# Optimization experiments

Hardware: AMD Instinct MI355X
Metric: run time of the kernel (lower is better)

Reference implementation:

```python
import jax, jax.numpy as jnp
import numpy as np

B, SW, SS, D, H = 2, 1024, 256, 1024, 16  # D = hidden_dim*num_heads = 64*16


def _dense_init(key, d_in, d_out):
    # xavier_uniform kernel, zero bias
    lim = np.sqrt(6.0 / (d_in + d_out))
    k = jax.random.uniform(key, (d_in, d_out), jnp.float32, -lim, lim)
    b = jnp.zeros((d_out,), jnp.float32)
    return k, b


def setup_inputs() -> dict:
    key = jax.random.key(0)
    ks = jax.random.split(key, 16)
    inp = {
        'word_inputs': jax.random.normal(ks[0], (B, SW, D), jnp.float32),
        'word_context': jax.random.normal(ks[1], (B, SW, D), jnp.float32),
        'sentence_inputs': jax.random.normal(ks[2], (B, SS, D), jnp.float32),
        'sentence_context': jax.random.normal(ks[3], (B, SS, D), jnp.float32),
        'word_mask': jax.random.uniform(ks[4], (B, H, SW, SW), jnp.float32),
        'sentence_mask': jax.random.uniform(ks[5], (B, H, SS, SS), jnp.float32),
    }
    names = ['wq', 'wk', 'wv', 'wo', 'sq', 'sk', 'sv', 'so']
    for i, n in enumerate(names):
        kk, bb = _dense_init(ks[6 + i], D, D)
        inp[n + '_k'] = kk
        inp[n + '_b'] = bb
    return inp


def _attention(q, k, v, mask):
    # Faithful to source: split heads by raw reshape (B, H, L, hd),
    # scale by sqrt(full key dim), multiplicative mask.
    Bq, Lk, Dm = v.shape[0], v.shape[1], q.shape[-1]
    hd = Dm // H
    qh = jnp.reshape(q, (Bq, H, Lk, hd))
    kh = jnp.reshape(k, (Bq, H, Lk, hd))
    vh = jnp.reshape(v, (Bq, H, Lk, hd))
    scores = jnp.einsum('bhqd,bhkd->bhqk', qh, kh) / jnp.sqrt(jnp.float32(Dm))
    if mask is not None:
        scores = scores * mask
    attn = jax.nn.softmax(scores, axis=-1)
    ctx = jnp.einsum('bhqk,bhkd->bhqd', attn, vh)
    return attn, jnp.reshape(ctx, (Bq, Lk, Dm))


def reference(word_inputs, word_context, sentence_inputs, sentence_context,
              word_mask, sentence_mask,
              wq_k, wq_b, wk_k, wk_b, wv_k, wv_b, wo_k, wo_b,
              sq_k, sq_b, sk_k, sk_b, sv_k, sv_b, so_k, so_b):
    dense = lambda x, k, b: jnp.einsum('bld,de->ble', x, k) + b
    wq = dense(word_inputs, wq_k, wq_b)
    wk = dense(word_context, wk_k, wk_b)
    wv = dense(word_context, wv_k, wv_b)
    word_attn, word_ctx = _attention(wq, wk, wv, word_mask)
    sq = dense(sentence_inputs, sq_k, sq_b)
    sk = dense(sentence_context, sk_k, sk_b)
    sv = dense(sentence_context, sv_k, sv_b)
    sent_attn, sent_ctx = _attention(sq, sk, sv, sentence_mask)
    word_out = dense(word_ctx, wo_k, wo_b)
    sent_out = dense(sent_ctx, so_k, so_b)
    return (word_out, sent_out, word_attn, sent_attn)
```

## Files before the change

### kernel.cpp

```cpp
#include <hip/hip_runtime.h>
#include <hip/hip_bf16.h>
#include <stdint.h>

typedef __attribute__((ext_vector_type(8))) short short8;
typedef __attribute__((ext_vector_type(4))) float f32x4;

__device__ __forceinline__ f32x4 mfma16(short8 a, short8 b, f32x4 c){
  return __builtin_amdgcn_mfma_f32_16x16x32_bf16(a, b, c, 0, 0, 0);
}

union BF8 { short8 v; __hip_bfloat16 h[8]; };

__device__ __forceinline__ void gld_lds16(const void* g, void* l){
  __builtin_amdgcn_global_load_lds((const __attribute__((address_space(1))) void*)g,
                                   (__attribute__((address_space(3))) void*)l, 16, 0, 0);
}

struct GemmDesc { const __hip_bfloat16* A; const __hip_bfloat16* W; const float* bias; void* out; int M; float scale; };
struct GemmArgs { GemmDesc d[6]; };
struct PrepWArgs { const float* src[8]; };
struct CvtArgs { const float* src[4]; __hip_bfloat16* dst[4]; int n[4]; };

__global__ __launch_bounds__(256) void cvt_k(CvtArgs c){
  int z = blockIdx.z;
  int n = c.n[z];
  int i = (blockIdx.x * 256 + threadIdx.x) * 8;
  if (i >= n) return;
  const float4* s = (const float4*)(c.src[z] + i);
  float4 u0 = s[0], u1 = s[1];
  BF8 cv;
  cv.h[0] = __float2bfloat16(u0.x); cv.h[1] = __float2bfloat16(u0.y);
  cv.h[2] = __float2bfloat16(u0.z); cv.h[3] = __float2bfloat16(u0.w);
  cv.h[4] = __float2bfloat16(u1.x); cv.h[5] = __float2bfloat16(u1.y);
  cv.h[6] = __float2bfloat16(u1.z); cv.h[7] = __float2bfloat16(u1.w);
  *(short8*)(c.dst[z] + i) = cv.v;
}

__global__ __launch_bounds__(256) void prep_w_k(PrepWArgs pa, __hip_bfloat16* dst){
  __shared__ float t[64][65];
  const float* W = pa.src[blockIdx.z];
  int k0 = blockIdx.y * 64, n0 = blockIdx.x * 64;
  int c = threadIdx.x & 63, r0 = (threadIdx.x >> 6) * 16;
  #pragma unroll
  for (int i = 0; i < 16; ++i) t[r0 + i][c] = W[(size_t)(k0 + r0 + i) * 1024 + n0 + c];
  __syncthreads();
  __hip_bfloat16* D = dst + (size_t)blockIdx.z * 1048576;
  #pragma unroll
  for (int i = 0; i < 16; ++i) D[(size_t)(n0 + r0 + i) * 1024 + k0 + c] = __float2bfloat16(t[c][r0 + i]);
}

__global__ __launch_bounds__(256) void prep_v_k(const __hip_bfloat16* vw, const __hip_bfloat16* vs,
                                                __hip_bfloat16* vtw, __hip_bfloat16* vts){
  bool word = (blockIdx.z == 0);
  int L = word ? 1024 : 256;
  if (!word && blockIdx.x >= 4) return;
  __shared__ __hip_bfloat16 t[64][65];
  const __hip_bfloat16* src = (word ? vw : vs) + (size_t)blockIdx.y * L * 64;
  __hip_bfloat16* dst = (word ? vtw : vts) + (size_t)blockIdx.y * L * 64;
  int l0 = blockIdx.x * 64;
  int c = threadIdx.x & 63, r0 = (threadIdx.x >> 6) * 16;
  #pragma unroll
  for (int i = 0; i < 16; ++i) t[r0 + i][c] = src[(size_t)(l0 + r0 + i) * 64 + c];
  __syncthreads();
  #pragma unroll
  for (int i = 0; i < 16; ++i) dst[(size_t)(r0 + i) * L + l0 + c] = t[c][r0 + i];
}

template<bool OUT_BF16>
__global__ __launch_bounds__(256) void gemm_k(GemmArgs ga){
  GemmDesc dd = ga.d[blockIdx.z];
  int m0 = blockIdx.y * 128;
  if (m0 >= dd.M) return;
  int n0 = blockIdx.x * 128;

  __shared__ __align__(16) __hip_bfloat16 lA[2][128 * 32];
  __shared__ __align__(16) __hip_bfloat16 lB[2][128 * 32];

  int tid = threadIdx.x, lane = tid & 63, wv = tid >> 6;
  int r16 = lane & 15, g = lane >> 4;
  int wr = wv >> 1, wc = wv & 1;

  const __hip_bfloat16* Ab = dd.A + (size_t)m0 * 1024;
  const __hip_bfloat16* Wb = dd.W + (size_t)n0 * 1024;
  int lrow = lane >> 2;
  int scol = (lane & 3) * 8;

  #define STAGE(buf, kc)                                                            \
    {                                                                               \
      _Pragma("unroll")                                                             \
      for (int h = 0; h < 2; ++h){                                                  \
        int rbase = h * 64 + wv * 16;                                               \
        int row = rbase + lrow;                                                     \
        gld_lds16(Ab + (size_t)row * 1024 + (kc) + scol, &lA[buf][rbase * 32]);     \
        gld_lds16(Wb + (size_t)row * 1024 + (kc) + scol, &lB[buf][rbase * 32]);     \
      }                                                                             \
    }

  f32x4 acc[4][4] = {};
  STAGE(0, 0);
  int cur = 0;
  for (int kc = 0; kc < 1024; kc += 32){
    if (kc + 32 < 1024) STAGE(cur ^ 1, kc + 32);
    __syncthreads();
    const __hip_bfloat16* la = &lA[cur][(wr * 64) * 32];
    const __hip_bfloat16* lb = &lB[cur][(wc * 64) * 32];
    short8 af[4], bfr[4];
    #pragma unroll
    for (int t = 0; t < 4; ++t){
      af[t]  = *(const short8*)(la + (t * 16 + r16) * 32 + g * 8);
      bfr[t] = *(const short8*)(lb + (t * 16 + r16) * 32 + g * 8);
    }
    #pragma unroll
    for (int mt = 0; mt < 4; ++mt)
      #pragma unroll
      for (int nt = 0; nt < 4; ++nt)
        acc[mt][nt] = mfma16(af[mt], bfr[nt], acc[mt][nt]);
    __syncthreads();
    cur ^= 1;
  }
  #undef STAGE

  #pragma unroll
  for (int nt = 0; nt < 4; ++nt){
    int col = n0 + wc * 64 + nt * 16 + r16;
    float bb = dd.bias[col];
    #pragma unroll
    for (int mt = 0; mt < 4; ++mt){
      int row0 = m0 + wr * 64 + mt * 16 + g * 4;
      #pragma unroll
      for (int r = 0; r < 4; ++r){
        float v = (acc[mt][nt][r] + bb) * dd.scale;
        if (OUT_BF16) ((__hip_bfloat16*)dd.out)[(size_t)(row0 + r) * 1024 + col] = __float2bfloat16(v);
        else          ((float*)dd.out)[(size_t)(row0 + r) * 1024 + col] = v;
      }
    }
  }
}

template<int L>
__global__ __launch_bounds__(512, 3) void attn_k(
    const __hip_bfloat16* __restrict__ qb, const __hip_bfloat16* __restrict__ kb,
    const __hip_bfloat16* __restrict__ vt, const float* __restrict__ mask,
    float* __restrict__ attn, __hip_bfloat16* __restrict__ ctx){
  constexpr int KQ = L / 4, KT = KQ / 16, CH = KQ / 32;
  int bh = blockIdx.y;
  int q0 = blockIdx.x * 32;
  int lane = threadIdx.x & 63, wv = threadIdx.x >> 6;
  int qt = wv >> 2, kq = wv & 3;
  int r16 = lane & 15, g = lane >> 4;
  size_t ho = (size_t)bh * L * 64;
  const __hip_bfloat16* Qp = qb + ho;
  const __hip_bfloat16* Kp = kb + ho + (size_t)kq * KQ * 64;
  const __hip_bfloat16* Vp = vt + ho;
  int q = q0 + qt * 16 + r16;
  const float* mrow = mask + (size_t)bh * L * L + (size_t)q * L + kq * KQ;
  float* arow = attn + (size_t)bh * L * L + (size_t)q * L + kq * KQ;

  short8 qf0 = *(const short8*)(Qp + (size_t)q * 64 + g * 8);
  short8 qf1 = *(const short8*)(Qp + (size_t)q * 64 + 32 + g * 8);

  f32x4 s[KT];
  #pragma unroll
  for (int kt = 0; kt < KT; ++kt){
    const __hip_bfloat16* kr = Kp + (size_t)(kt * 16 + r16) * 64 + g * 8;
    short8 kf0 = *(const short8*)kr;
    short8 kf1 = *(const short8*)(kr + 32);
    f32x4 t = {};
    t = mfma16(kf0, qf0, t);
    t = mfma16(kf1, qf1, t);
    float4 mv = *(const float4*)(mrow + kt * 16 + g * 4);
    t[0] *= mv.x; t[1] *= mv.y; t[2] *= mv.z; t[3] *= mv.w;
    s[kt] = t;
  }

  float mx = -3.0e38f;
  #pragma unroll
  for (int kt = 0; kt < KT; ++kt)
    #pragma unroll
    for (int r = 0; r < 4; ++r) mx = fmaxf(mx, s[kt][r]);
  mx = fmaxf(mx, __shfl_xor(mx, 16));
  mx = fmaxf(mx, __shfl_xor(mx, 32));
  __shared__ float redm[2][4][16], redl[2][4][16];
  if (lane < 16) redm[qt][kq][lane] = mx;
  __syncthreads();
  mx = fmaxf(fmaxf(redm[qt][0][r16], redm[qt][1][r16]),
             fmaxf(redm[qt][2][r16], redm[qt][3][r16]));
  float sm = 0.f;
  #pragma unroll
  for (int kt = 0; kt < KT; ++kt)
    #pragma unroll
    for (int r = 0; r < 4; ++r){ float e = __expf(s[kt][r] - mx); s[kt][r] = e; sm += e; }
  sm += __shfl_xor(sm, 16);
  sm += __shfl_xor(sm, 32);
  if (lane < 16) redl[qt][kq][lane] = sm;
  __syncthreads();
  sm = (redl[qt][0][r16] + redl[qt][1][r16]) + (redl[qt][2][r16] + redl[qt][3][r16]);
  float inv = 1.0f / sm;

  #pragma unroll
  for (int kt = 0; kt < KT; ++kt){
    float4 v;
    v.x = s[kt][0] * inv; v.y = s[kt][1] * inv;
    v.z = s[kt][2] * inv; v.w = s[kt][3] * inv;
    s[kt][0] = v.x; s[kt][1] = v.y; s[kt][2] = v.z; s[kt][3] = v.w;
    *(float4*)(arow + kt * 16 + g * 4) = v;
  }

  __shared__ __align__(16) __hip_bfloat16 plds[8][16][40];
  f32x4 c4[4] = {};
  #pragma unroll
  for (int ch = 0; ch < CH; ++ch){
    asm volatile("s_waitcnt lgkmcnt(0)" ::: "memory");
    #pragma unroll
    for (int t = 0; t < 2; ++t){
      union { uint64_t u; __hip_bfloat16 h[4]; } pk;
      pk.h[0] = __float2bfloat16(s[2 * ch + t][0]);
      pk.h[1] = __float2bfloat16(s[2 * ch + t][1]);
      pk.h[2] = __float2bfloat16(s[2 * ch + t][2]);
      pk.h[3] = __float2bfloat16(s[2 * ch + t][3]);
      *(uint64_t*)&plds[wv][r16][t * 16 + g * 4] = pk.u;
    }
    asm volatile("s_waitcnt lgkmcnt(0)" ::: "memory");
    __builtin_amdgcn_sched_barrier(0);
    short8 pf = *(const short8*)&plds[wv][r16][g * 8];
    const __hip_bfloat16* vpp = Vp + kq * KQ + ch * 32 + g * 8;
    #pragma unroll
    for (int nt = 0; nt < 4; ++nt){
      short8 vf = *(const short8*)(vpp + (size_t)(nt * 16 + r16) * L);
      c4[nt] = mfma16(pf, vf, c4[nt]);
    }
  }

  __shared__ float ctxl[2][4][16][65];
  #pragma unroll
  for (int nt = 0; nt < 4; ++nt)
    #pragma unroll
    for (int r = 0; r < 4; ++r) ctxl[qt][kq][g * 4 + r][nt * 16 + r16] = c4[nt][r];
  __syncthreads();
  {
    int dq = kq * 16 + g * 4;
    union { uint64_t u; __hip_bfloat16 h[4]; } ov;
    #pragma unroll
    for (int rr = 0; rr < 4; ++rr){
      float v = (ctxl[qt][0][r16][dq + rr] + ctxl[qt][1][r16][dq + rr]) +
                (ctxl[qt][2][r16][dq + rr] + ctxl[qt][3][r16][dq + rr]);
      ov.h[rr] = __float2bfloat16(v);
    }
    *(uint64_t*)(ctx + ho + (size_t)(q0 + qt * 16 + r16) * 64 + dq) = ov.u;
  }
}

extern "C" void kernel_launch(void* const* d_in, const int* in_sizes, int n_in,
                              void* d_out, int out_size, void* d_ws, size_t ws_size,
                              hipStream_t stream){
  const float* word_mask = (const float*)d_in[4];
  const float* sent_mask = (const float*)d_in[5];

  char* ws = (char*)d_ws;
  const size_t MB = 1048576;
  __hip_bfloat16* Wt   = (__hip_bfloat16*)(ws);
  __hip_bfloat16* bwi  = (__hip_bfloat16*)(ws + 16 * MB);
  __hip_bfloat16* bwc  = (__hip_bfloat16*)(ws + 20 * MB);
  __hip_bfloat16* bsi  = (__hip_bfloat16*)(ws + 24 * MB);
  __hip_bfloat16* bsc  = (__hip_bfloat16*)(ws + 25 * MB);
  __hip_bfloat16* qw   = (__hip_bfloat16*)(ws + 26 * MB);
  __hip_bfloat16* kw   = (__hip_bfloat16*)(ws + 30 * MB);
  __hip_bfloat16* vw   = (__hip_bfloat16*)(ws + 34 * MB);
  __hip_bfloat16* sqb  = (__hip_bfloat16*)(ws + 38 * MB);
  __hip_bfloat16* skb  = (__hip_bfloat16*)(ws + 39 * MB);
  __hip_bfloat16* svb  = (__hip_bfloat16*)(ws + 40 * MB);
  __hip_bfloat16* vtw  = (__hip_bfloat16*)(ws + 41 * MB);
  __hip_bfloat16* vts  = (__hip_bfloat16*)(ws + 45 * MB);
  __hip_bfloat16* ctxw = (__hip_bfloat16*)(ws + 46 * MB);
  __hip_bfloat16* ctxs = (__hip_bfloat16*)(ws + 50 * MB);

  float* out = (float*)d_out;
  float* word_out  = out;
  float* sent_out  = out + 2097152;
  float* word_attn = out + 2621440;
  float* sent_attn = out + 36175872;

  PrepWArgs pw;
  pw.src[0] = (const float*)d_in[6];  pw.src[1] = (const float*)d_in[8];
  pw.src[2] = (const float*)d_in[10]; pw.src[3] = (const float*)d_in[12];
  pw.src[4] = (const float*)d_in[14]; pw.src[5] = (const float*)d_in[16];
  pw.src[6] = (const float*)d_in[18]; pw.src[7] = (const float*)d_in[20];
  prep_w_k<<<dim3(16, 16, 8), 256, 0, stream>>>(pw, Wt);

  CvtArgs cv;
  cv.src[0] = (const float*)d_in[0]; cv.dst[0] = bwi; cv.n[0] = 2097152;
  cv.src[1] = (const float*)d_in[1]; cv.dst[1] = bwc; cv.n[1] = 2097152;
  cv.src[2] = (const float*)d_in[2]; cv.dst[2] = bsi; cv.n[2] = 524288;
  cv.src[3] = (const float*)d_in[3]; cv.dst[3] = bsc; cv.n[3] = 524288;
  cvt_k<<<dim3(1024, 1, 4), 256, 0, stream>>>(cv);

  GemmArgs g1;
  g1.d[0] = { bwi, Wt + (size_t)0 * 1048576, (const float*)d_in[7],  qw,  2048, 1.0f / 32.0f };
  g1.d[1] = { bwc, Wt + (size_t)1 * 1048576, (const float*)d_in[9],  kw,  2048, 1.0f };
  g1.d[2] = { bwc, Wt + (size_t)2 * 1048576, (const float*)d_in[11], vw,  2048, 1.0f };
  g1.d[3] = { bsi, Wt + (size_t)4 * 1048576, (const float*)d_in[15], sqb, 512,  1.0f / 32.0f };
  g1.d[4] = { bsc, Wt + (size_t)5 * 1048576, (const float*)d_in[17], skb, 512,  1.0f };
  g1.d[5] = { bsc, Wt + (size_t)6 * 1048576, (const float*)d_in[19], svb, 512,  1.0f };
  gemm_k<true><<<dim3(8, 16, 6), 256, 0, stream>>>(g1);

  prep_v_k<<<dim3(16, 32, 2), 256, 0, stream>>>(vw, svb, vtw, vts);

  attn_k<1024><<<dim3(32, 32), 512, 0, stream>>>(qw, kw, vtw, word_mask, word_attn, ctxw);
  attn_k<256><<<dim3(8, 32), 512, 0, stream>>>(sqb, skb, vts, sent_mask, sent_attn, ctxs);

  GemmArgs g2 = {};
  g2.d[0] = { ctxw, Wt + (size_t)3 * 1048576, (const float*)d_in[13], word_out, 2048, 1.0f };
  g2.d[1] = { ctxs, Wt + (size_t)7 * 1048576, (const float*)d_in[21], sent_out, 512,  1.0f };
  gemm_k<false><<<dim3(8, 16, 2), 256, 0, stream>>>(g2);
}
```

Baseline: 200.4 us.

## Software-pipeline K, mask and V loads in attention kernel

Restructures the attention kernel's QK^T loop to prefetch K fragments four tiles ahead in a ring buffer and batch mask loads in groups of eight. The PV loop double-buffers V fragments one chunk ahead and drops the explicit lgkmcnt waits and sched barrier around the LDS round-trip. Occupancy hint drops from 3 to 2 blocks per SM to make room for the extra registers. The goal is to hide global load latency; risks are register pressure, lower occupancy, and relying on the compiler to order the LDS write and read correctly.

```diff
diff --git a/kernel.cpp b/kernel.cpp
--- a/kernel.cpp
+++ b/kernel.cpp
@@ -138,11 +138,12 @@
 }
 
 template<int L>
-__global__ __launch_bounds__(512, 3) void attn_k(
+__global__ __launch_bounds__(512, 2) void attn_k(
     const __hip_bfloat16* __restrict__ qb, const __hip_bfloat16* __restrict__ kb,
     const __hip_bfloat16* __restrict__ vt, const float* __restrict__ mask,
     float* __restrict__ attn, __hip_bfloat16* __restrict__ ctx){
   constexpr int KQ = L / 4, KT = KQ / 16, CH = KQ / 32;
+  constexpr int MC = (KT < 8) ? KT : 8;
   int bh = blockIdx.y;
   int q0 = blockIdx.x * 32;
   int lane = threadIdx.x & 63, wv = threadIdx.x >> 6;
@@ -160,17 +161,34 @@
   short8 qf1 = *(const short8*)(Qp + (size_t)q * 64 + 32 + g * 8);
 
   f32x4 s[KT];
-  #pragma unroll
-  for (int kt = 0; kt < KT; ++kt){
-    const __hip_bfloat16* kr = Kp + (size_t)(kt * 16 + r16) * 64 + g * 8;
-    short8 kf0 = *(const short8*)kr;
-    short8 kf1 = *(const short8*)(kr + 32);
-    f32x4 t = {};
-    t = mfma16(kf0, qf0, t);
-    t = mfma16(kf1, qf1, t);
-    float4 mv = *(const float4*)(mrow + kt * 16 + g * 4);
-    t[0] *= mv.x; t[1] *= mv.y; t[2] *= mv.z; t[3] *= mv.w;
-    s[kt] = t;
+  short8 kfa[4], kfb[4];
+  #pragma unroll
+  for (int p = 0; p < 4 && p < KT; ++p){
+    const __hip_bfloat16* kr = Kp + (size_t)(p * 16 + r16) * 64 + g * 8;
+    kfa[p] = *(const short8*)kr;
+    kfb[p] = *(const short8*)(kr + 32);
+  }
+  #pragma unroll
+  for (int h2 = 0; h2 < KT / MC; ++h2){
+    float4 mv[MC];
+    #pragma unroll
+    for (int j = 0; j < MC; ++j)
+      mv[j] = *(const float4*)(mrow + (h2 * MC + j) * 16 + g * 4);
+    #pragma unroll
+    for (int j = 0; j < MC; ++j){
+      int kt = h2 * MC + j;
+      short8 a0 = kfa[kt & 3], a1 = kfb[kt & 3];
+      if (kt + 4 < KT){
+        const __hip_bfloat16* kr = Kp + (size_t)((kt + 4) * 16 + r16) * 64 + g * 8;
+        kfa[kt & 3] = *(const short8*)kr;
+        kfb[kt & 3] = *(const short8*)(kr + 32);
+      }
+      f32x4 t = {};
+      t = mfma16(a0, qf0, t);
+      t = mfma16(a1, qf1, t);
+      t[0] *= mv[j].x; t[1] *= mv[j].y; t[2] *= mv[j].z; t[3] *= mv[j].w;
+      s[kt] = t;
+    }
   }
 
   float mx = -3.0e38f;
@@ -208,9 +226,18 @@
 
   __shared__ __align__(16) __hip_bfloat16 plds[8][16][40];
   f32x4 c4[4] = {};
+  const __hip_bfloat16* vbase = Vp + kq * KQ;
+  short8 vf0[4], vf1[4];
+  #pragma unroll
+  for (int nt = 0; nt < 4; ++nt)
+    vf0[nt] = *(const short8*)(vbase + (size_t)(nt * 16 + r16) * L + g * 8);
   #pragma unroll
   for (int ch = 0; ch < CH; ++ch){
-    asm volatile("s_waitcnt lgkmcnt(0)" ::: "memory");
+    if (ch + 1 < CH){
+      #pragma unroll
+      for (int nt = 0; nt < 4; ++nt)
+        vf1[nt] = *(const short8*)(vbase + (ch + 1) * 32 + (size_t)(nt * 16 + r16) * L + g * 8);
+    }
     #pragma unroll
     for (int t = 0; t < 2; ++t){
       union { uint64_t u; __hip_bfloat16 h[4]; } pk;
@@ -220,15 +247,12 @@
       pk.h[3] = __float2bfloat16(s[2 * ch + t][3]);
       *(uint64_t*)&plds[wv][r16][t * 16 + g * 4] = pk.u;
     }
-    asm volatile("s_waitcnt lgkmcnt(0)" ::: "memory");
-    __builtin_amdgcn_sched_barrier(0);
     short8 pf = *(const short8*)&plds[wv][r16][g * 8];
-    const __hip_bfloat16* vpp = Vp + kq * KQ + ch * 32 + g * 8;
-    #pragma unroll
-    for (int nt = 0; nt < 4; ++nt){
-      short8 vf = *(const short8*)(vpp + (size_t)(nt * 16 + r16) * L);
-      c4[nt] = mfma16(pf, vf, c4[nt]);
-    }
+    #pragma unroll
+    for (int nt = 0; nt < 4; ++nt)
+      c4[nt] = mfma16(pf, vf0[nt], c4[nt]);
+    #pragma unroll
+    for (int nt = 0; nt < 4; ++nt) vf0[nt] = vf1[nt];
   }
 
   __shared__ float ctxl[2][4][16][65];
```

Measured after the change: 202.4 us. No clear change (+1.0%).

## Split attention keys across eight waves per 16-query block with nontemporal mask/attn

Applied to the files above, without the earlier changes.

Each attention block now handles 16 queries, and all eight waves split the key dimension into eighths, replacing the earlier split of two query tiles by four key quarters. The grid doubles and the launch-bounds occupancy hint rises from 3 to 6 to raise parallelism and latency hiding. The mask load and attention-probability store use nontemporal builtins so these streaming accesses are meant to bypass cache retention. The manual waitcnt/sched_barrier around the P tile in LDS is removed, which leaves ordering to the compiler. The cross-wave reductions and context sum now combine eight partials, adding LDS reduction work and register pressure under the tighter bound.

```diff
diff --git a/kernel.cpp b/kernel.cpp
--- a/kernel.cpp
+++ b/kernel.cpp
@@ -138,21 +138,20 @@
 }
 
 template<int L>
-__global__ __launch_bounds__(512, 3) void attn_k(
+__global__ __launch_bounds__(512, 6) void attn_k(
     const __hip_bfloat16* __restrict__ qb, const __hip_bfloat16* __restrict__ kb,
     const __hip_bfloat16* __restrict__ vt, const float* __restrict__ mask,
     float* __restrict__ attn, __hip_bfloat16* __restrict__ ctx){
-  constexpr int KQ = L / 4, KT = KQ / 16, CH = KQ / 32;
+  constexpr int KQ = L / 8, KT = KQ / 16, CH = KQ / 32;
   int bh = blockIdx.y;
-  int q0 = blockIdx.x * 32;
-  int lane = threadIdx.x & 63, wv = threadIdx.x >> 6;
-  int qt = wv >> 2, kq = wv & 3;
+  int q0 = blockIdx.x * 16;
+  int lane = threadIdx.x & 63, kq = threadIdx.x >> 6;
   int r16 = lane & 15, g = lane >> 4;
   size_t ho = (size_t)bh * L * 64;
   const __hip_bfloat16* Qp = qb + ho;
   const __hip_bfloat16* Kp = kb + ho + (size_t)kq * KQ * 64;
   const __hip_bfloat16* Vp = vt + ho;
-  int q = q0 + qt * 16 + r16;
+  int q = q0 + r16;
   const float* mrow = mask + (size_t)bh * L * L + (size_t)q * L + kq * KQ;
   float* arow = attn + (size_t)bh * L * L + (size_t)q * L + kq * KQ;
 
@@ -168,8 +167,8 @@
     f32x4 t = {};
     t = mfma16(kf0, qf0, t);
     t = mfma16(kf1, qf1, t);
-    float4 mv = *(const float4*)(mrow + kt * 16 + g * 4);
-    t[0] *= mv.x; t[1] *= mv.y; t[2] *= mv.z; t[3] *= mv.w;
+    f32x4 mv = __builtin_nontemporal_load((const f32x4*)(mrow + kt * 16 + g * 4));
+    t[0] *= mv[0]; t[1] *= mv[1]; t[2] *= mv[2]; t[3] *= mv[3];
     s[kt] = t;
   }
 
@@ -180,11 +179,11 @@
     for (int r = 0; r < 4; ++r) mx = fmaxf(mx, s[kt][r]);
   mx = fmaxf(mx, __shfl_xor(mx, 16));
   mx = fmaxf(mx, __shfl_xor(mx, 32));
-  __shared__ float redm[2][4][16], redl[2][4][16];
-  if (lane < 16) redm[qt][kq][lane] = mx;
-  __syncthreads();
-  mx = fmaxf(fmaxf(redm[qt][0][r16], redm[qt][1][r16]),
-             fmaxf(redm[qt][2][r16], redm[qt][3][r16]));
+  __shared__ float redm[8][16], redl[8][16];
+  if (lane < 16) redm[kq][lane] = mx;
+  __syncthreads();
+  mx = fmaxf(fmaxf(fmaxf(redm[0][r16], redm[1][r16]), fmaxf(redm[2][r16], redm[3][r16])),
+             fmaxf(fmaxf(redm[4][r16], redm[5][r16]), fmaxf(redm[6][r16], redm[7][r16])));
   float sm = 0.f;
   #pragma unroll
   for (int kt = 0; kt < KT; ++kt)
@@ -192,25 +191,26 @@
     for (int r = 0; r < 4; ++r){ float e = __expf(s[kt][r] - mx); s[kt][r] = e; sm += e; }
   sm += __shfl_xor(sm, 16);
   sm += __shfl_xor(sm, 32);
-  if (lane < 16) redl[qt][kq][lane] = sm;
-  __syncthreads();
-  sm = (redl[qt][0][r16] + redl[qt][1][r16]) + (redl[qt][2][r16] + redl[qt][3][r16]);
+  if (lane < 16) redl[kq][lane] = sm;
+  __syncthreads();
+  sm = ((redl[0][r16] + redl[1][r16]) + (redl[2][r16] + redl[3][r16])) +
+       ((redl[4][r16] + redl[5][r16]) + (redl[6][r16] + redl[7][r16]));
   float inv = 1.0f / sm;
 
   #pragma unroll
   for (int kt = 0; kt < KT; ++kt){
-    float4 v;
-    v.x = s[kt][0] * inv; v.y = s[kt][1] * inv;
-    v.z = s[kt][2] * inv; v.w = s[kt][3] * inv;
-    s[kt][0] = v.x; s[kt][1] = v.y; s[kt][2] = v.z; s[kt][3] = v.w;
-    *(float4*)(arow + kt * 16 + g * 4) = v;
+    f32x4 v;
+    v[0] = s[kt][0] * inv; v[1] = s[kt][1] * inv;
+    v[2] = s[kt][2] * inv; v[3] = s[kt][3] * inv;
+    s[kt] = v;
+    __builtin_nontemporal_store(v, (f32x4*)(arow + kt * 16 + g * 4));
   }
 
   __shared__ __align__(16) __hip_bfloat16 plds[8][16][40];
   f32x4 c4[4] = {};
+  const __hip_bfloat16* vbase = Vp + kq * KQ;
   #pragma unroll
   for (int ch = 0; ch < CH; ++ch){
-    asm volatile("s_waitcnt lgkmcnt(0)" ::: "memory");
     #pragma unroll
     for (int t = 0; t < 2; ++t){
       union { uint64_t u; __hip_bfloat16 h[4]; } pk;
@@ -218,12 +218,10 @@
       pk.h[1] = __float2bfloat16(s[2 * ch + t][1]);
       pk.h[2] = __float2bfloat16(s[2 * ch + t][2]);
       pk.h[3] = __float2bfloat16(s[2 * ch + t][3]);
-      *(uint64_t*)&plds[wv][r16][t * 16 + g * 4] = pk.u;
-    }
-    asm volatile("s_waitcnt lgkmcnt(0)" ::: "memory");
-    __builtin_amdgcn_sched_barrier(0);
-    short8 pf = *(const short8*)&plds[wv][r16][g * 8];
-    const __hip_bfloat16* vpp = Vp + kq * KQ + ch * 32 + g * 8;
+      *(uint64_t*)&plds[kq][r16][t * 16 + g * 4] = pk.u;
+    }
+    short8 pf = *(const short8*)&plds[kq][r16][g * 8];
+    const __hip_bfloat16* vpp = vbase + ch * 32 + g * 8;
     #pragma unroll
     for (int nt = 0; nt < 4; ++nt){
       short8 vf = *(const short8*)(vpp + (size_t)(nt * 16 + r16) * L);
@@ -231,22 +229,24 @@
     }
   }
 
-  __shared__ float ctxl[2][4][16][65];
+  __shared__ float ctxl[8][16][65];
   #pragma unroll
   for (int nt = 0; nt < 4; ++nt)
     #pragma unroll
-    for (int r = 0; r < 4; ++r) ctxl[qt][kq][g * 4 + r][nt * 16 + r16] = c4[nt][r];
-  __syncthreads();
-  {
+    for (int r = 0; r < 4; ++r) ctxl[kq][g * 4 + r][nt * 16 + r16] = c4[nt][r];
+  __syncthreads();
+  if (kq < 4){
     int dq = kq * 16 + g * 4;
     union { uint64_t u; __hip_bfloat16 h[4]; } ov;
     #pragma unroll
     for (int rr = 0; rr < 4; ++rr){
-      float v = (ctxl[qt][0][r16][dq + rr] + ctxl[qt][1][r16][dq + rr]) +
-                (ctxl[qt][2][r16][dq + rr] + ctxl[qt][3][r16][dq + rr]);
+      float v = ((ctxl[0][r16][dq + rr] + ctxl[1][r16][dq + rr]) +
+                 (ctxl[2][r16][dq + rr] + ctxl[3][r16][dq + rr])) +
+                ((ctxl[4][r16][dq + rr] + ctxl[5][r16][dq + rr]) +
+                 (ctxl[6][r16][dq + rr] + ctxl[7][r16][dq + rr]));
       ov.h[rr] = __float2bfloat16(v);
     }
-    *(uint64_t*)(ctx + ho + (size_t)(q0 + qt * 16 + r16) * 64 + dq) = ov.u;
+    *(uint64_t*)(ctx + ho + (size_t)(q0 + r16) * 64 + dq) = ov.u;
   }
 }
 
@@ -305,8 +305,8 @@
 
   prep_v_k<<<dim3(16, 32, 2), 256, 0, stream>>>(vw, svb, vtw, vts);
 
-  attn_k<1024><<<dim3(32, 32), 512, 0, stream>>>(qw, kw, vtw, word_mask, word_attn, ctxw);
-  attn_k<256><<<dim3(8, 32), 512, 0, stream>>>(sqb, skb, vts, sent_mask, sent_attn, ctxs);
+  attn_k<1024><<<dim3(64, 32), 512, 0, stream>>>(qw, kw, vtw, word_mask, word_attn, ctxw);
+  attn_k<256><<<dim3(16, 32), 512, 0, stream>>>(sqb, skb, vts, sent_mask, sent_attn, ctxs);
 
   GemmArgs g2 = {};
   g2.d[0] = { ctxw, Wt + (size_t)3 * 1048576, (const float*)d_in[13], word_out, 2048, 1.0f };
```

After: 211.0 us. 1.05x slower.
